# Optimization experiments

Measured on AMD Instinct MI355X. Metric: run time of the kernel, lower is better.

The kernel has to match this reference:

```python
import jax, jax.numpy as jnp
import numpy as np
import math

K = 30   # neighbors
T = 9    # num_kernel

def sparsemax(z):
    # sparsemax along last axis
    zs = jnp.sort(z, axis=-1)[..., ::-1]
    rng = jnp.arange(1, z.shape[-1] + 1, dtype=z.dtype)
    cs = jnp.cumsum(zs, axis=-1)
    support = (1.0 + rng * zs) > cs
    kz = jnp.sum(support, axis=-1, keepdims=True)
    tau = (jnp.take_along_axis(cs, kz - 1, axis=-1) - 1.0) / kz.astype(z.dtype)
    return jnp.maximum(z - tau, 0.0)

def bn(x, g, b, axes, eps=1e-5):
    # batch-norm (training-mode batch stats), channel axis = 1
    m = jnp.mean(x, axes, keepdims=True)
    v = jnp.var(x, axes, keepdims=True)
    sh = [1] * x.ndim; sh[1] = -1
    return (x - m) / jnp.sqrt(v + eps) * g.reshape(sh) + b.reshape(sh)

def _forward(x, B_ff, mlp_W, permx, W1, b1, S1, W2, b2, S2, W3, b3, S3, W4, b4, S4,
             W5, g5, be5, L1, g6, be6, L2, bL2, g7, be7, L3, bL3):
    Bsz, _, N = x.shape
    pts = jnp.transpose(x, (0, 2, 1))                      # [B,N,3]
    # knn (DGCNN-style): negative squared distance, top-k (self first)
    xx = jnp.sum(pts * pts, -1)                            # [B,N]
    inner = jnp.einsum('bnc,bmc->bnm', pts, pts)
    negd = 2.0 * inner - xx[:, :, None] - xx[:, None, :]
    _, idx = jax.lax.top_k(negd, K)                        # [B,N,K] int32
    gather = jax.vmap(lambda f, i: f[i])                   # [B,N,F],[B,N,K]->[B,N,K,F]
    # Fourier features -> sparsemax basis weights -> per-point permatrix
    ng = gather(pts, idx)                                  # [B,N,K,3]
    xrep = jnp.broadcast_to(ng[:, :, :1, :], ng.shape)     # self repeated
    rel = ng - xrep
    sq = jnp.sum(rel * rel, -1, keepdims=True)
    dist = jnp.where(sq > 0, jnp.sqrt(jnp.where(sq > 0, sq, 1.0)), 0.0)  # safe norm
    feats = jnp.concatenate([xrep, rel, dist], -1).reshape(Bsz, N, 7 * K)
    ff = (2.0 * math.pi) * (feats @ B_ff)                  # [B,N,32]
    ff = jnp.concatenate([jnp.sin(ff), jnp.cos(ff)], -1)   # [B,N,64]
    w = sparsemax(ff @ mlp_W)                              # [B,N,16]
    P = jnp.einsum('bni,ikt->bnkt', w, permx)              # [B,N,K,T]

    def paiconv(f, W, b, S):  # f: [B,Cin,N]
        ft = jnp.transpose(f, (0, 2, 1))                   # [B,N,Cin]
        nb = gather(ft, idx)                               # [B,N,K,Cin]
        agg = jnp.einsum('bnkc,bnkt->bntc', nb, P).reshape(Bsz, N, -1)
        out = agg @ W + b + ft @ S                         # [B,N,Cout]
        return jnp.transpose(out, (0, 2, 1))

    gelu = lambda a: jax.nn.gelu(a, approximate=False)
    x1 = gelu(paiconv(x,  W1, b1, S1))
    x2 = gelu(paiconv(x1, W2, b2, S2))
    x3 = gelu(paiconv(x2, W3, b3, S3))
    x4 = gelu(paiconv(x3, W4, b4, S4))
    f = jnp.concatenate([x1, x2, x3, x4], 1)               # [B,512,N]
    f = jnp.einsum('bcn,ce->ben', f, W5)                   # conv5 (1x1)
    f = gelu(bn(f, g5, be5, (0, 2)))
    h = jnp.concatenate([jnp.max(f, -1), jnp.mean(f, -1)], -1)  # [B,2048]
    h = gelu(bn(h @ L1, g6, be6, (0,)))
    h = gelu(bn(h @ L2 + bL2, g7, be7, (0,)))
    return h @ L3 + bL3


def setup_inputs() -> dict:
    key = jax.random.key(0)
    ks = jax.random.split(key, 20)
    rn = lambda k_, sh, s=1.0: jax.random.normal(k_, sh, dtype=jnp.float32) * s
    B, N = 16, 1024
    inp = {}
    inp['x'] = rn(ks[0], (B, 3, N))
    inp['B_ff'] = rn(ks[1], (7 * K, 32))
    inp['mlp_W'] = rn(ks[2], (64, 16), 0.125)
    inp['permx'] = rn(ks[3], (16, K, T), 0.1)
    dims = [(3, 64), (64, 64), (64, 128), (128, 256)]
    for i, (ci, co) in enumerate(dims, 1):
        inp['W%d' % i] = rn(ks[3 + i], (T * ci, co), 1.0 / float(np.sqrt(T * ci)))
        inp['b%d' % i] = jnp.zeros((co,), jnp.float32)
        inp['S%d' % i] = rn(ks[7 + i], (ci, co), 1.0 / float(np.sqrt(ci)))
    inp['W5'] = rn(ks[12], (512, 1024), 1.0 / float(np.sqrt(512)))
    inp['g5'] = jnp.ones((1024,), jnp.float32); inp['be5'] = jnp.zeros((1024,), jnp.float32)
    inp['L1'] = rn(ks[13], (2048, 512), 1.0 / float(np.sqrt(2048)))
    inp['g6'] = jnp.ones((512,), jnp.float32); inp['be6'] = jnp.zeros((512,), jnp.float32)
    inp['L2'] = rn(ks[14], (512, 256), 1.0 / float(np.sqrt(512))); inp['bL2'] = jnp.zeros((256,), jnp.float32)
    inp['g7'] = jnp.ones((256,), jnp.float32); inp['be7'] = jnp.zeros((256,), jnp.float32)
    inp['L3'] = rn(ks[15], (256, 40), 1.0 / float(np.sqrt(256))); inp['bL3'] = jnp.zeros((40,), jnp.float32)
    return inp


def reference(x, B_ff, mlp_W, permx, W1, b1, S1, W2, b2, S2, W3, b3, S3, W4, b4, S4,
              W5, g5, be5, L1, g6, be6, L2, bL2, g7, be7, L3, bL3):
    return _forward(x, B_ff, mlp_W, permx, W1, b1, S1, W2, b2, S2, W3, b3, S3, W4, b4, S4,
                    W5, g5, be5, L1, g6, be6, L2, bL2, g7, be7, L3, bL3)
```

## Files before the change

### kernel.cpp

```cpp
#include <hip/hip_runtime.h>
#include <hip/hip_bf16.h>
#include <cstddef>

#define BSZ 16
#define NPT 1024
#define KNN 30
#define TKR 9
#define FLT_BIG 3.402823466e+38f

typedef unsigned short u16;
typedef __attribute__((ext_vector_type(8))) u16 u16x8;
typedef __attribute__((ext_vector_type(4))) float f32x4;

__device__ __forceinline__ float gelu_f(float x) {
    return 0.5f * x * (1.0f + erff(x * 0.7071067811865476f));
}

__device__ __forceinline__ u16 bf16_rne(float a) {
    unsigned u = __float_as_uint(a);
    u += 0x7FFFu + ((u >> 16) & 1u);
    return (u16)(u >> 16);
}
__device__ __forceinline__ float bf16_tof(u16 h) {
    return __uint_as_float(((unsigned)h) << 16);
}
__device__ __forceinline__ void split_bf16(float a, u16& h, u16& l) {
    h = bf16_rne(a);
    float r = a - bf16_tof(h);
    l = bf16_rne(r);
}

__device__ __forceinline__ size_t pack_off(int row, int k, int npanels_row) {
    return (size_t)((k >> 5) * npanels_row + (row >> 7)) * 4096
         + (size_t)(((k >> 3) & 3) * 1024 + (row & 127) * 8 + (k & 7));
}

__global__ __launch_bounds__(256) void prep_all(
    const float* __restrict__ x, float* __restrict__ pts,
    const float* __restrict__ W1, const float* __restrict__ S1, float* __restrict__ wz1,
    const float* __restrict__ W2, const float* __restrict__ S2, float* __restrict__ wz2,
    const float* __restrict__ W3, const float* __restrict__ S3, float* __restrict__ wz3,
    const float* __restrict__ W4, const float* __restrict__ S4,
    u16* __restrict__ w4tH, u16* __restrict__ w4tL) {
    int layer = blockIdx.y;
    int t = blockIdx.x * 256 + threadIdx.x;
    if (layer == 0) {
        if (t >= BSZ * NPT) return;
        int b = t >> 10, n = t & 1023;
        const float* xp = x + (size_t)b * 3 * NPT;
        pts[t * 3 + 0] = xp[n];
        pts[t * 3 + 1] = xp[NPT + n];
        pts[t * 3 + 2] = xp[2 * NPT + n];
        return;
    }
    if (layer == 4) {
        if (t >= 1280 * 256) return;
        int k = t >> 8, n = t & 255;
        float v = (k < 1152) ? W4[(size_t)k * 256 + n] : S4[(size_t)(k - 1152) * 256 + n];
        u16 h, l;
        split_bf16(v, h, l);
        size_t off = pack_off(n, k, 2);
        w4tH[off] = h;
        w4tL[off] = l;
        return;
    }
    const float *W, *S; float* WZ; int KW, KS, N, kpad;
    if (layer == 1)      { W = W1; S = S1; WZ = wz1; KW = 27;   KS = 3;   N = 64;  kpad = 32;  }
    else if (layer == 2) { W = W2; S = S2; WZ = wz2; KW = 576;  KS = 64;  N = 64;  kpad = 640; }
    else                 { W = W3; S = S3; WZ = wz3; KW = 576;  KS = 64;  N = 128; kpad = 640; }
    if (t >= kpad * N) return;
    int k = t / N, n = t - k * N;
    float v = 0.0f;
    if (k < KW) v = W[(size_t)k * N + n];
    else if (k < KW + KS) v = S[(size_t)(k - KW) * N + n];
    WZ[t] = v;
}

__global__ __launch_bounds__(256) void knn_basis_kernel(
    const float* __restrict__ pts, const float* __restrict__ B_ff,
    const float* __restrict__ mlp_W, const float* __restrict__ permx,
    int* __restrict__ idx, float* __restrict__ P) {
    __shared__ float npt[4][KNN * 3];
    __shared__ float feats[4][7 * KNN];
    __shared__ float sc[4][64];
    __shared__ float zl[4][16];
    __shared__ float w[4][16];
    __shared__ float sZs[4][16];
    __shared__ float sCs[4][16];
    __shared__ int sIds[4][KNN];
    int tid = threadIdx.x;
    int wave = tid >> 6, lane = tid & 63;
    int bn_ = blockIdx.x * 4 + wave;
    int b = bn_ >> 10;

    {
        double px = (double)pts[(size_t)bn_ * 3 + 0];
        double py = (double)pts[(size_t)bn_ * 3 + 1];
        double pz = (double)pts[(size_t)bn_ * 3 + 2];
        double xn = px * px + py * py + pz * pz;
        const float* pb = pts + (size_t)(b << 10) * 3;
        int base = lane * 16;
        unsigned mono[16];
        #pragma unroll
        for (int j = 0; j < 16; j++) {
            int m = base + j;
            double qx = (double)pb[m * 3 + 0];
            double qy = (double)pb[m * 3 + 1];
            double qz = (double)pb[m * 3 + 2];
            double inner = px * qx + py * qy + pz * qz;
            double xm = qx * qx + qy * qy + qz * qz;
            double cd = 2.0 * inner - xn - xm;
            float cf = (float)cd;
            unsigned bb = __float_as_uint(cf);
            mono[j] = (bb & 0x80000000u) ? ~bb : (bb | 0x80000000u);
        }
        unsigned alive = 0xFFFFu;
        unsigned c1v = 0u, c2v = 0u;
        int c1j = 0, c2j = 0;
        #pragma unroll
        for (int j = 0; j < 16; j++) {
            unsigned v = mono[j];
            if (v > c1v) { c2v = c1v; c2j = c1j; c1v = v; c1j = j; }
            else if (v > c2v) { c2v = v; c2j = j; }
        }
        bool have2 = true;
        for (int it = 0; it < KNN; it++) {
            unsigned m = c1v;
            #pragma unroll
            for (int s = 1; s < 64; s <<= 1) {
                unsigned ov = (unsigned)__shfl_xor((int)m, s, 64);
                m = (ov > m) ? ov : m;
            }
            unsigned long long ball = __ballot(c1v == m);
            int wlan = (int)__builtin_ctzll(ball);
            int jw = __shfl(c1j, wlan, 64);
            int bi = (wlan << 4) + jw;
            if (lane == it) sIds[wave][it] = bi;
            if (lane == wlan) {
                alive &= ~(1u << c1j);
                if (have2) {
                    c1v = c2v; c1j = c2j; have2 = false;
                } else {
                    unsigned a1 = 0u, a2 = 0u;
                    int j1 = 0, j2 = 0;
                    #pragma unroll
                    for (int j = 0; j < 16; j++) {
                        unsigned v = ((alive >> j) & 1u) ? mono[j] : 0u;
                        if (v > a1) { a2 = a1; j2 = j1; a1 = v; j1 = j; }
                        else if (v > a2) { a2 = v; j2 = j; }
                    }
                    c1v = a1; c1j = j1; c2v = a2; c2j = j2;
                    have2 = true;
                }
            }
        }
        __builtin_amdgcn_wave_barrier();
        if (lane < KNN) idx[(size_t)bn_ * KNN + lane] = sIds[wave][lane];
    }
    __syncthreads();

    if (lane < KNN) {
        int m = sIds[wave][lane];
        const float* q = pts + ((size_t)(b << 10) + m) * 3;
        npt[wave][lane * 3 + 0] = q[0];
        npt[wave][lane * 3 + 1] = q[1];
        npt[wave][lane * 3 + 2] = q[2];
    }
    __syncthreads();
    if (lane < KNN) {
        float sx = npt[wave][0], sy = npt[wave][1], sz = npt[wave][2];
        float rx = npt[wave][lane * 3 + 0] - sx;
        float ry = npt[wave][lane * 3 + 1] - sy;
        float rz = npt[wave][lane * 3 + 2] - sz;
        float sq = rx * rx + ry * ry + rz * rz;
        float dist = (sq > 0.0f) ? sqrtf(sq) : 0.0f;
        feats[wave][lane * 7 + 0] = sx;
        feats[wave][lane * 7 + 1] = sy;
        feats[wave][lane * 7 + 2] = sz;
        feats[wave][lane * 7 + 3] = rx;
        feats[wave][lane * 7 + 4] = ry;
        feats[wave][lane * 7 + 5] = rz;
        feats[wave][lane * 7 + 6] = dist;
    }
    __syncthreads();
    {
        int j = lane & 31;
        int half = lane >> 5;
        int i0 = half * 105;
        float acc = 0.0f;
        for (int i = i0; i < i0 + 105; i++) acc += feats[wave][i] * B_ff[i * 32 + j];
        acc += __shfl_xor(acc, 32, 64);
        if (half == 0) {
            float ffv = 6.283185307179586f * acc;
            sc[wave][j] = sinf(ffv);
            sc[wave][j + 32] = cosf(ffv);
        }
    }
    __syncthreads();
    {
        int j = lane & 15;
        int h = lane >> 4;
        float acc = 0.0f;
        for (int i = 16 * h; i < 16 * h + 16; i++) acc += sc[wave][i] * mlp_W[i * 16 + j];
        acc += __shfl_xor(acc, 16, 64);
        acc += __shfl_xor(acc, 32, 64);
        if (h == 0) zl[wave][j] = acc;
    }
    __syncthreads();
    {
        int l = lane & 15;
        float zv = zl[wave][l];
        int rank = 0;
        #pragma unroll
        for (int j = 0; j < 16; j++) {
            float zj = zl[wave][j];
            rank += (zj > zv || (zj == zv && j < l)) ? 1 : 0;
        }
        if (lane < 16) sZs[wave][rank] = zv;
        __builtin_amdgcn_wave_barrier();
        float cs = 0.0f;
        #pragma unroll
        for (int p = 0; p < 16; p++) {
            float zp = sZs[wave][p];
            cs += (p <= l) ? zp : 0.0f;
        }
        float zsl = sZs[wave][l];
        bool flag = (lane < 16) && (1.0f + (float)(l + 1) * zsl > cs);
        unsigned long long ball = __ballot(flag);
        int cnt = (int)__popcll(ball & 0xFFFFull);
        if (lane < 16) sCs[wave][l] = cs;
        __builtin_amdgcn_wave_barrier();
        float tau = (sCs[wave][cnt - 1] - 1.0f) / (float)cnt;
        if (lane < 16) w[wave][l] = fmaxf(zv - tau, 0.0f);
    }
    __syncthreads();
    float* Pp = P + (size_t)bn_ * (KNN * TKR);
    for (int e = lane; e < KNN * TKR; e += 64) {
        int k = e / TKR, t = e - TKR * k;
        float acc = 0.0f;
        for (int i = 0; i < 16; i++) acc += w[wave][i] * permx[(i * KNN + k) * TKR + t];
        Pp[e] = acc;
    }
}

template <int CIN>
__global__ __launch_bounds__(256) void agg_kernel(
    const float* __restrict__ ft, int ftst,
    const float* __restrict__ P, const int* __restrict__ idx,
    float* __restrict__ Z, int kpad) {
    __shared__ float sP[KNN * TKR];
    __shared__ float sNb[KNN * CIN];
    __shared__ int sIdx[KNN];
    int bn_ = blockIdx.x;
    int b = bn_ >> 10;
    int tid = threadIdx.x;
    if (tid < KNN) sIdx[tid] = idx[(size_t)bn_ * KNN + tid];
    for (int e = tid; e < KNN * TKR; e += 256) sP[e] = P[(size_t)bn_ * (KNN * TKR) + e];
    __syncthreads();
    for (int e = tid; e < KNN * CIN; e += 256) {
        int k = e / CIN, c = e - k * CIN;
        sNb[e] = ft[((size_t)(b << 10) + sIdx[k]) * ftst + c];
    }
    __syncthreads();
    float* zp = Z + (size_t)bn_ * kpad;
    const int KW = TKR * CIN;
    for (int e = tid; e < kpad; e += 256) {
        float v;
        if (e < KW) {
            int t = e / CIN, c = e - t * CIN;
            float acc = 0.0f;
            #pragma unroll
            for (int k = 0; k < KNN; k++) acc += sNb[k * CIN + c] * sP[k * TKR + t];
            v = acc;
        } else if (e < KW + CIN) {
            v = ft[(size_t)bn_ * ftst + (e - KW)];
        } else {
            v = 0.0f;
        }
        zp[e] = v;
    }
}

template <int CIN>
__global__ __launch_bounds__(256) void agg_v_kernel(
    const float* __restrict__ ft, int ftst,
    const float* __restrict__ P, const int* __restrict__ idx,
    float* __restrict__ Z, int kpad) {
    __shared__ float sP[KNN * TKR];
    __shared__ float sNb[KNN * CIN];
    __shared__ int sIdx[KNN];
    constexpr int C4 = CIN / 4;
    int bn_ = blockIdx.x;
    int b = bn_ >> 10;
    int tid = threadIdx.x;
    if (tid < KNN) sIdx[tid] = idx[(size_t)bn_ * KNN + tid];
    for (int e = tid; e < KNN * TKR; e += 256) sP[e] = P[(size_t)bn_ * (KNN * TKR) + e];
    __syncthreads();
    for (int e = tid; e < KNN * C4; e += 256) {
        int k = e / C4, c4 = (e - k * C4) * 4;
        *(float4*)&sNb[k * CIN + c4] =
            *(const float4*)&ft[((size_t)(b << 10) + sIdx[k]) * ftst + c4];
    }
    __syncthreads();
    float* zp = Z + (size_t)bn_ * kpad;
    const int KW = TKR * CIN;
    for (int e = tid; e < (kpad >> 2); e += 256) {
        int c0 = e * 4;
        float4 v;
        if (c0 < KW) {
            int t = c0 / CIN, c4 = c0 - t * CIN;
            float4 a = make_float4(0.f, 0.f, 0.f, 0.f);
            #pragma unroll
            for (int k = 0; k < KNN; k++) {
                float p = sP[k * TKR + t];
                float4 nb = *(const float4*)&sNb[k * CIN + c4];
                a.x += nb.x * p; a.y += nb.y * p;
                a.z += nb.z * p; a.w += nb.w * p;
            }
            v = a;
        } else if (c0 < KW + CIN) {
            v = *(const float4*)&ft[(size_t)bn_ * ftst + (c0 - KW)];
        } else {
            v = make_float4(0.f, 0.f, 0.f, 0.f);
        }
        *(float4*)&zp[c0] = v;
    }
}

__global__ __launch_bounds__(256) void agg_v_split8_kernel(
    const float* __restrict__ ft, int ftst,
    const float* __restrict__ P, const int* __restrict__ idx,
    u16* __restrict__ ZH, u16* __restrict__ ZL) {
    __shared__ int   sIdx8[8][KNN];
    __shared__ float sP8[8][KNN * TKR];
    __shared__ __align__(16) u16 oH[8][1288];
    __shared__ __align__(16) u16 oL[8][1288];
    int tid = threadIdx.x;
    int row = tid >> 5;
    int cq = tid & 31;
    int c0 = cq << 2;
    int r0 = blockIdx.x << 3;
    int b = r0 >> 10;

    if (tid < 8 * KNN) {
        int r = tid / KNN, k = tid - r * KNN;
        sIdx8[r][k] = idx[(size_t)(r0 + r) * KNN + k];
    }
    for (int e = tid; e < 8 * KNN * TKR; e += 256) {
        int r = e / (KNN * TKR), i = e - r * (KNN * TKR);
        sP8[r][i] = P[(size_t)(r0 + r) * (KNN * TKR) + i];
    }
    __syncthreads();

    float4 acc[9];
    #pragma unroll
    for (int t = 0; t < 9; t++) acc[t] = make_float4(0.f, 0.f, 0.f, 0.f);
    const float* fb = ft + (size_t)(b << 10) * ftst;
    for (int k = 0; k < KNN; k++) {
        float4 nb = *(const float4*)&fb[(size_t)sIdx8[row][k] * ftst + c0];
        #pragma unroll
        for (int t = 0; t < 9; t++) {
            float p = sP8[row][k * TKR + t];
            acc[t].x += nb.x * p; acc[t].y += nb.y * p;
            acc[t].z += nb.z * p; acc[t].w += nb.w * p;
        }
    }
    float4 self = *(const float4*)&ft[(size_t)(r0 + row) * ftst + c0];

    #pragma unroll
    for (int t = 0; t < 10; t++) {
        float4 v = (t < 9) ? acc[t] : self;
        int e0 = (t < 9) ? (t * 128 + c0) : (1152 + c0);
        u16 h[4], l[4];
        split_bf16(v.x, h[0], l[0]);
        split_bf16(v.y, h[1], l[1]);
        split_bf16(v.z, h[2], l[2]);
        split_bf16(v.w, h[3], l[3]);
        uint2 hv, lv;
        hv.x = (unsigned)h[0] | ((unsigned)h[1] << 16);
        hv.y = (unsigned)h[2] | ((unsigned)h[3] << 16);
        lv.x = (unsigned)l[0] | ((unsigned)l[1] << 16);
        lv.y = (unsigned)l[2] | ((unsigned)l[3] << 16);
        *(uint2*)&oH[row][e0] = hv;
        *(uint2*)&oL[row][e0] = lv;
    }
    __syncthreads();

    for (int u = tid; u < 2560; u += 256) {
        int kp = u >> 6;
        int l = u & 63;
        int kc = l >> 4, rg = (l >> 3) & 1, rw = (l >> 1) & 3, half = l & 1;
        int rloc = rg * 4 + rw;
        int eloc = kp * 32 + kc * 8 + half * 4;
        uint2 hv = *(const uint2*)&oH[rloc][eloc];
        uint2 lv = *(const uint2*)&oL[rloc][eloc];
        size_t off = (size_t)(kp * 128 + (r0 >> 7)) * 4096
                   + (size_t)(kc * 1024 + ((r0 & 127) + rloc) * 8 + half * 4);
        *(uint2*)&ZH[off] = hv;
        *(uint2*)&ZL[off] = lv;
    }
}

template <bool GELU, bool HASBIAS>
__global__ __launch_bounds__(256) void gemm_f32_64db(
    const float* __restrict__ A, int lda,
    const float* __restrict__ B, int ldb, int K,
    const float* __restrict__ bias,
    float* __restrict__ C, int ldc) {
    __shared__ float As[2][16][64];
    __shared__ float Bs[2][16][64];
    int tid = threadIdx.x;
    int tx = tid & 15, ty = tid >> 4;
    int m0 = blockIdx.y * 64, n0 = blockIdx.x * 64;
    float acc[4][4];
    #pragma unroll
    for (int i = 0; i < 4; i++)
        #pragma unroll
        for (int j = 0; j < 4; j++) acc[i][j] = 0.0f;

    int ar = tid >> 2, ac0 = (tid & 3) * 4;
    const float* aptr = A + (size_t)(m0 + ar) * lda + ac0;
    int br = tid >> 4, bc = (tid & 15) * 4;
    const float* bptr = B + (size_t)br * ldb + n0 + bc;

    float4 pa = *(const float4*)(aptr);
    float4 pb = *(const float4*)(bptr);
    As[0][ac0 + 0][ar] = pa.x; As[0][ac0 + 1][ar] = pa.y;
    As[0][ac0 + 2][ar] = pa.z; As[0][ac0 + 3][ar] = pa.w;
    *(float4*)&Bs[0][br][bc] = pb;
    __syncthreads();

    int nk = K >> 4;
    for (int t = 0; t < nk; t++) {
        int buf = t & 1;
        bool more = (t + 1) < nk;
        if (more) {
            int k0 = (t + 1) << 4;
            pa = *(const float4*)(aptr + k0);
            pb = *(const float4*)(bptr + (size_t)k0 * ldb);
        }
        #pragma unroll
        for (int kk = 0; kk < 16; kk++) {
            float av[4], bv[4];
            *(float4*)&av[0] = *(const float4*)&As[buf][kk][ty * 4];
            *(float4*)&bv[0] = *(const float4*)&Bs[buf][kk][tx * 4];
            #pragma unroll
            for (int i = 0; i < 4; i++)
                #pragma unroll
                for (int j = 0; j < 4; j++) acc[i][j] += av[i] * bv[j];
        }
        if (more) {
            int nb = 1 - buf;
            As[nb][ac0 + 0][ar] = pa.x; As[nb][ac0 + 1][ar] = pa.y;
            As[nb][ac0 + 2][ar] = pa.z; As[nb][ac0 + 3][ar] = pa.w;
            *(float4*)&Bs[nb][br][bc] = pb;
        }
        __syncthreads();
    }
    #pragma unroll
    for (int i = 0; i < 4; i++) {
        int r = m0 + ty * 4 + i;
        int c = n0 + tx * 4;
        float v[4];
        #pragma unroll
        for (int j = 0; j < 4; j++) {
            float t = acc[i][j];
            if (HASBIAS) t += bias[c + j];
            if (GELU) t = gelu_f(t);
            v[j] = t;
        }
        *(float4*)(C + (size_t)r * ldc + c) = *(float4*)v;
    }
}

__global__ __launch_bounds__(256) void convert_split(
    const float* __restrict__ feat, u16* __restrict__ fH, u16* __restrict__ fL,
    const float* __restrict__ W5, u16* __restrict__ wH, u16* __restrict__ wL) {
    int t = blockIdx.x * 256 + threadIdx.x;
    if (blockIdx.y == 0) {
        int T = t >> 9, s = t & 511;
        int kc = s >> 7, rloc = s & 127;
        int kp = T >> 7, rp = T & 127;
        int row = (rp << 7) + rloc;
        int k0 = (kp << 5) + (kc << 3);
        const float* fp = &feat[(size_t)row * 512 + k0];
        float4 a = *(const float4*)fp;
        float4 b = *(const float4*)(fp + 4);
        float v[8] = {a.x, a.y, a.z, a.w, b.x, b.y, b.z, b.w};
        u16 h[8], l[8];
        #pragma unroll
        for (int i = 0; i < 8; i++) split_bf16(v[i], h[i], l[i]);
        uint4 hv, lv;
        hv.x = (unsigned)h[0] | ((unsigned)h[1] << 16);
        hv.y = (unsigned)h[2] | ((unsigned)h[3] << 16);
        hv.z = (unsigned)h[4] | ((unsigned)h[5] << 16);
        hv.w = (unsigned)h[6] | ((unsigned)h[7] << 16);
        lv.x = (unsigned)l[0] | ((unsigned)l[1] << 16);
        lv.y = (unsigned)l[2] | ((unsigned)l[3] << 16);
        lv.z = (unsigned)l[4] | ((unsigned)l[5] << 16);
        lv.w = (unsigned)l[6] | ((unsigned)l[7] << 16);
        size_t off = (size_t)T * 4096 + kc * 1024 + rloc * 8;
        *(uint4*)&fH[off] = hv;
        *(uint4*)&fL[off] = lv;
    } else {
        if (t >= 512 * 1024) return;
        int n = t >> 9, k = t & 511;
        u16 h, l;
        split_bf16(W5[(size_t)k * 1024 + n], h, l);
        size_t off = pack_off(n, k, 8);
        wH[off] = h; wL[off] = l;
    }
}

template <bool STATS, bool GELU, bool HASBIAS>
__global__ __launch_bounds__(256) void mfma_bf16x3(
    const u16* __restrict__ fH, const u16* __restrict__ fL,
    const u16* __restrict__ wH, const u16* __restrict__ wL,
    int K, const float* __restrict__ bias,
    float* __restrict__ C, int ldc,
    float* __restrict__ partS, float* __restrict__ partQ) {
    __shared__ __align__(16) u16 lds[2][16384];
    int tid = threadIdx.x;
    int lane = tid & 63, wave = tid >> 6;
    int wr = wave >> 1, wc = wave & 1;
    int kg = lane >> 4, r = lane & 15;

    int nwg = gridDim.x * gridDim.y;
    int hw = blockIdx.y * gridDim.x + blockIdx.x;
    int logical = (hw & 7) * (nwg >> 3) + (hw >> 3);
    int nb = logical % gridDim.x;
    int mb = logical / gridDim.x;
    int m0 = mb << 7, n0 = nb << 7;
    int nmp = gridDim.y;
    int nnp = gridDim.x;

    const u16* src = (wave == 0) ? fH : (wave == 1) ? fL
                   : (wave == 2) ? wH : wL;

    f32x4 acc[4][4];
    #pragma unroll
    for (int i = 0; i < 4; i++)
        #pragma unroll
        for (int j = 0; j < 4; j++) {
            acc[i][j][0] = 0.0f; acc[i][j][1] = 0.0f;
            acc[i][j][2] = 0.0f; acc[i][j][3] = 0.0f;
        }

#define STAGE_K(BUF, TT) {                                                     \
    size_t tb = ((size_t)((wave < 2) ? ((TT) * nmp + mb)                       \
                                     : ((TT) * nnp + nb)) << 12);              \
    _Pragma("unroll")                                                          \
    for (int iw = 0; iw < 8; iw++) {                                           \
        const u16* gp = src + tb + (size_t)(((iw << 6) + lane) << 3);          \
        __builtin_amdgcn_global_load_lds(                                      \
            (const __attribute__((address_space(1))) void*)gp,                 \
            (__attribute__((address_space(3))) void*)&lds[BUF][(wave << 12) + (iw << 9)], \
            16, 0, 0);                                                         \
    } }

    int nk = K >> 5;
    STAGE_K(0, 0);
    __syncthreads();
    for (int t = 0; t < nk; t++) {
        if (t + 1 < nk) STAGE_K((t + 1) & 1, (t + 1));
        const u16* lb = lds[t & 1];
        u16x8 bh[4], bl[4];
        #pragma unroll
        for (int fj = 0; fj < 4; fj++) {
            int bcol = (wc << 6) + (fj << 4) + r;
            bh[fj] = *(const u16x8*)&lb[ 8192 + (((kg << 7) + bcol) << 3)];
            bl[fj] = *(const u16x8*)&lb[12288 + (((kg << 7) + bcol) << 3)];
        }
        #pragma unroll
        for (int fi = 0; fi < 4; fi++) {
            int arow = (wr << 6) + (fi << 4) + r;
            u16x8 ah = *(const u16x8*)&lb[       (((kg << 7) + arow) << 3)];
            u16x8 al = *(const u16x8*)&lb[4096 + (((kg << 7) + arow) << 3)];
            #pragma unroll
            for (int fj = 0; fj < 4; fj++) {
                asm volatile("v_mfma_f32_16x16x32_bf16 %0, %1, %2, %0"
                             : "+v"(acc[fi][fj]) : "v"(ah), "v"(bh[fj]));
                asm volatile("v_mfma_f32_16x16x32_bf16 %0, %1, %2, %0"
                             : "+v"(acc[fi][fj]) : "v"(ah), "v"(bl[fj]));
                asm volatile("v_mfma_f32_16x16x32_bf16 %0, %1, %2, %0"
                             : "+v"(acc[fi][fj]) : "v"(al), "v"(bh[fj]));
            }
        }
        __syncthreads();
    }
#undef STAGE_K

    asm volatile("s_nop 15\n\ts_nop 15" ::: "memory");

    float bvv[4];
    if (HASBIAS) {
        #pragma unroll
        for (int fj = 0; fj < 4; fj++) bvv[fj] = bias[n0 + (wc << 6) + (fj << 4) + r];
    }

    #pragma unroll
    for (int fi = 0; fi < 4; fi++)
        #pragma unroll
        for (int ri = 0; ri < 4; ri++) {
            int row = m0 + (wr << 6) + (fi << 4) + (kg << 2) + ri;
            float* cp = C + (size_t)row * ldc + n0 + (wc << 6) + r;
            #pragma unroll
            for (int fj = 0; fj < 4; fj++) {
                float v = acc[fi][fj][ri];
                if (HASBIAS) v += bvv[fj];
                if (GELU) v = gelu_f(v);
                cp[fj << 4] = v;
            }
        }

    if (STATS) {
        __syncthreads();
        float* sS = (float*)lds;
        float* sQ = sS + 1024;
        int slot = (wr << 2) + kg;
        #pragma unroll
        for (int fj = 0; fj < 4; fj++) {
            float s = 0.0f, q = 0.0f;
            #pragma unroll
            for (int fi = 0; fi < 4; fi++)
                #pragma unroll
                for (int ri = 0; ri < 4; ri++) {
                    float v = acc[fi][fj][ri];
                    s += v; q += v * v;
                }
            int cl = (wc << 6) + (fj << 4) + r;
            sS[slot * 128 + cl] = s;
            sQ[slot * 128 + cl] = q;
        }
        __syncthreads();
        if (tid < 128) {
            float S = 0.0f, Q = 0.0f;
            #pragma unroll
            for (int i = 0; i < 8; i++) { S += sS[i * 128 + tid]; Q += sQ[i * 128 + tid]; }
            partS[(size_t)mb * 1024 + n0 + tid] = S;
            partQ[(size_t)mb * 1024 + n0 + tid] = Q;
        }
    }
}

__global__ __launch_bounds__(256) void stats_reduce(
    const float* __restrict__ partS, const float* __restrict__ partQ,
    const float* __restrict__ g, const float* __restrict__ be,
    float* __restrict__ scaleb, float* __restrict__ shiftb) {
    int e = blockIdx.x * 256 + threadIdx.x;
    if (e >= 1024) return;
    double s = 0.0, q = 0.0;
    for (int mb = 0; mb < 128; mb++) {
        s += (double)partS[(size_t)mb * 1024 + e];
        q += (double)partQ[(size_t)mb * 1024 + e];
    }
    double m = s * (1.0 / 16384.0);
    double v = q * (1.0 / 16384.0) - m * m;
    float sc = g[e] * (float)(1.0 / sqrt(v + 1e-5));
    scaleb[e] = sc;
    shiftb[e] = be[e] - (float)m * sc;
}

__global__ __launch_bounds__(256) void pool_partial(
    const float* __restrict__ f5, const float* __restrict__ scaleb,
    const float* __restrict__ shiftb,
    float* __restrict__ partM, double* __restrict__ partSd) {
    int chunk = blockIdx.x, g = blockIdx.y, b = blockIdx.z;
    int tid = threadIdx.x;
    int lane = tid & 63, nlane = tid >> 6;
    int c0 = (g << 8) + lane * 4;
    float4 sc = *(const float4*)&scaleb[c0];
    float4 sh = *(const float4*)&shiftb[c0];
    float m0 = -FLT_BIG, m1 = -FLT_BIG, m2 = -FLT_BIG, m3 = -FLT_BIG;
    double s0 = 0.0, s1 = 0.0, s2 = 0.0, s3 = 0.0;
    int nend = (chunk + 1) << 6;
    for (int n = (chunk << 6) + nlane; n < nend; n += 4) {
        float4 v = *(const float4*)&f5[((size_t)(b << 10) + n) * 1024 + c0];
        float g0 = gelu_f(v.x * sc.x + sh.x);
        float g1 = gelu_f(v.y * sc.y + sh.y);
        float g2 = gelu_f(v.z * sc.z + sh.z);
        float g3 = gelu_f(v.w * sc.w + sh.w);
        m0 = fmaxf(m0, g0); m1 = fmaxf(m1, g1);
        m2 = fmaxf(m2, g2); m3 = fmaxf(m3, g3);
        s0 += (double)g0; s1 += (double)g1;
        s2 += (double)g2; s3 += (double)g3;
    }
    __shared__ float smax[4][256];
    __shared__ double ssum[4][256];
    *(float4*)&smax[nlane][lane * 4] = make_float4(m0, m1, m2, m3);
    ssum[nlane][lane * 4 + 0] = s0;
    ssum[nlane][lane * 4 + 1] = s1;
    ssum[nlane][lane * 4 + 2] = s2;
    ssum[nlane][lane * 4 + 3] = s3;
    __syncthreads();
    if (nlane == 0) {
        size_t base = ((size_t)((b * 4 + g) * 16 + chunk)) * 256 + lane * 4;
        #pragma unroll
        for (int j = 0; j < 4; j++) {
            float mm = smax[0][lane * 4 + j];
            double ss = ssum[0][lane * 4 + j];
            #pragma unroll
            for (int i = 1; i < 4; i++) {
                mm = fmaxf(mm, smax[i][lane * 4 + j]);
                ss += ssum[i][lane * 4 + j];
            }
            partM[base + j] = mm;
            partSd[base + j] = ss;
        }
    }
}

__global__ __launch_bounds__(256) void pool_finish(
    const float* __restrict__ partM, const double* __restrict__ partSd,
    float* __restrict__ h) {
    int b = blockIdx.x;
    int e0 = threadIdx.x * 4;
    int g = e0 >> 8, cl = e0 & 255;
    float mm[4] = {-FLT_BIG, -FLT_BIG, -FLT_BIG, -FLT_BIG};
    double ss[4] = {0.0, 0.0, 0.0, 0.0};
    for (int chunk = 0; chunk < 16; chunk++) {
        size_t base = ((size_t)((b * 4 + g) * 16 + chunk)) * 256 + cl;
        float4 pm = *(const float4*)&partM[base];
        mm[0] = fmaxf(mm[0], pm.x); mm[1] = fmaxf(mm[1], pm.y);
        mm[2] = fmaxf(mm[2], pm.z); mm[3] = fmaxf(mm[3], pm.w);
        ss[0] += partSd[base + 0]; ss[1] += partSd[base + 1];
        ss[2] += partSd[base + 2]; ss[3] += partSd[base + 3];
    }
    #pragma unroll
    for (int j = 0; j < 4; j++) {
        h[(size_t)b * 2048 + e0 + j] = mm[j];
        h[(size_t)b * 2048 + 1024 + e0 + j] = (float)(ss[j] * (1.0 / 1024.0));
    }
}

__global__ __launch_bounds__(256) void fc_split(
    const float* __restrict__ X, const float* __restrict__ W,
    double* __restrict__ part, int Bn, int In, int Out, int KC) {
    int tid = blockIdx.x * 256 + threadIdx.x;
    if (tid >= Bn * Out * KC) return;
    int chunk = tid / (Bn * Out);
    int r = tid - chunk * (Bn * Out);
    int b = r / Out, j = r - b * Out;
    int len = In / KC;
    int i0 = chunk * len;
    const float* x = X + (size_t)b * In + i0;
    const float* w = W + (size_t)i0 * Out + j;
    double acc = 0.0;
    for (int i = 0; i < len; i++) acc += (double)x[i] * (double)w[(size_t)i * Out];
    part[tid] = acc;
}

__global__ __launch_bounds__(256) void fc_bn_gelu(
    const double* __restrict__ part, const float* __restrict__ bias,
    const float* __restrict__ g, const float* __restrict__ be,
    float* __restrict__ Y, int Out, int KC) {
    int j = blockIdx.x * 256 + threadIdx.x;
    if (j >= Out) return;
    float r[BSZ];
    for (int b = 0; b < BSZ; b++) {
        double acc = bias ? (double)bias[j] : 0.0;
        for (int c = 0; c < KC; c++) acc += part[(size_t)c * (BSZ * Out) + b * Out + j];
        r[b] = (float)acc;
    }
    double m = 0.0;
    for (int b = 0; b < BSZ; b++) m += (double)r[b];
    m /= (double)BSZ;
    double v = 0.0;
    for (int b = 0; b < BSZ; b++) {
        double dd = (double)r[b] - m;
        v += dd * dd;
    }
    v /= (double)BSZ;
    float sc = g[j] * (float)(1.0 / sqrt(v + 1e-5));
    float sh = be[j] - (float)m * sc;
    for (int b = 0; b < BSZ; b++) Y[b * Out + j] = gelu_f(r[b] * sc + sh);
}

__global__ __launch_bounds__(256) void fc_reduce(
    const double* __restrict__ part, const float* __restrict__ bias,
    float* __restrict__ Y, int Bn, int Out, int KC) {
    int r = blockIdx.x * 256 + threadIdx.x;
    if (r >= Bn * Out) return;
    int j = r % Out;
    double acc = bias ? (double)bias[j] : 0.0;
    for (int c = 0; c < KC; c++) acc += part[(size_t)c * (Bn * Out) + r];
    Y[r] = (float)acc;
}

extern "C" void kernel_launch(void* const* d_in, const int* in_sizes, int n_in,
                              void* d_out, int out_size, void* d_ws, size_t ws_size,
                              hipStream_t stream) {
    const float* x     = (const float*)d_in[0];
    const float* B_ff  = (const float*)d_in[1];
    const float* mlp_W = (const float*)d_in[2];
    const float* permx = (const float*)d_in[3];
    const float* W1 = (const float*)d_in[4];
    const float* b1 = (const float*)d_in[5];
    const float* S1 = (const float*)d_in[6];
    const float* W2 = (const float*)d_in[7];
    const float* b2 = (const float*)d_in[8];
    const float* S2 = (const float*)d_in[9];
    const float* W3 = (const float*)d_in[10];
    const float* b3 = (const float*)d_in[11];
    const float* S3 = (const float*)d_in[12];
    const float* W4 = (const float*)d_in[13];
    const float* b4 = (const float*)d_in[14];
    const float* S4 = (const float*)d_in[15];
    const float* W5 = (const float*)d_in[16];
    const float* g5 = (const float*)d_in[17];
    const float* be5 = (const float*)d_in[18];
    const float* L1 = (const float*)d_in[19];
    const float* g6 = (const float*)d_in[20];
    const float* be6 = (const float*)d_in[21];
    const float* L2 = (const float*)d_in[22];
    const float* bL2 = (const float*)d_in[23];
    const float* g7 = (const float*)d_in[24];
    const float* be7 = (const float*)d_in[25];
    const float* L3 = (const float*)d_in[26];
    const float* bL3 = (const float*)d_in[27];
    float* outp = (float*)d_out;

    const int BN = BSZ * NPT;

    float* ws = (float*)d_ws;
    float* pts   = ws;
    int*   idxb  = (int*)(ws + 49152);
    float* Pb    = ws + 540672;
    float* feat  = Pb + 4423680;
    float* Zbig  = feat + 8388608;
    u16*   ZH    = (u16*)Zbig;
    u16*   ZL    = (u16*)(Zbig + 10485760);
    float* f5    = Zbig;
    u16*   featH = (u16*)(Zbig + 16777216);
    float* poolM = Zbig + 16777216;
    double* poolS = (double*)(Zbig + 16777216 + 262144);
    float* w4slot = Zbig + 20971520;
    u16*   w4tH  = (u16*)w4slot;
    u16*   w4tL  = w4tH + 327680;
    float* scb   = w4slot + 327680;
    float* shb   = scb + 1024;
    float* hb    = shb + 1024;
    float* y1    = hb + 32768;
    float* y2    = y1 + 8192;
    float* partC_S = y2 + 4096;
    float* partC_Q = partC_S + 131072;
    double* partF  = (double*)(partC_Q + 131072);
    float* wsend = (float*)(partF + 131072);
    u16* featL = (u16*)ws;
    u16* w5tH  = (u16*)(ws + 4194304);
    u16* w5tL  = (u16*)(ws + 4456448);
    float* wz1   = Zbig + 11010048;
    float* wz2   = wz1 + 2048;
    float* wz3   = wz2 + 40960;
    size_t need_bytes = (size_t)(wsend - ws) * sizeof(float);
    if (ws_size < need_bytes) return;

    prep_all<<<dim3(1280, 5), 256, 0, stream>>>(
        x, pts, W1, S1, wz1, W2, S2, wz2, W3, S3, wz3, W4, S4, w4tH, w4tL);

    knn_basis_kernel<<<BN / 4, 256, 0, stream>>>(pts, B_ff, mlp_W, permx, idxb, Pb);

    agg_kernel<3><<<BN, 256, 0, stream>>>(pts, 3, Pb, idxb, Zbig, 32);
    gemm_f32_64db<true, true><<<dim3(1, 256), 256, 0, stream>>>(
        Zbig, 32, wz1, 64, 32, b1, feat + 0, 512);
    agg_v_kernel<64><<<BN, 256, 0, stream>>>(feat + 0, 512, Pb, idxb, Zbig, 640);
    gemm_f32_64db<true, true><<<dim3(1, 256), 256, 0, stream>>>(
        Zbig, 640, wz2, 64, 640, b2, feat + 64, 512);
    agg_v_kernel<64><<<BN, 256, 0, stream>>>(feat + 64, 512, Pb, idxb, Zbig, 640);
    gemm_f32_64db<true, true><<<dim3(2, 256), 256, 0, stream>>>(
        Zbig, 640, wz3, 128, 640, b3, feat + 128, 512);
    agg_v_split8_kernel<<<BN / 8, 256, 0, stream>>>(feat + 128, 512, Pb, idxb, ZH, ZL);
    mfma_bf16x3<false, true, true><<<dim3(2, 128), 256, 0, stream>>>(
        ZH, ZL, w4tH, w4tL, 1280, b4, feat + 256, 512, nullptr, nullptr);

    convert_split<<<dim3(4096, 2), 256, 0, stream>>>(feat, featH, featL, W5, w5tH, w5tL);
    mfma_bf16x3<true, false, false><<<dim3(8, 128), 256, 0, stream>>>(
        featH, featL, w5tH, w5tL, 512, nullptr, f5, 1024, partC_S, partC_Q);

    stats_reduce<<<4, 256, 0, stream>>>(partC_S, partC_Q, g5, be5, scb, shb);
    pool_partial<<<dim3(16, 4, BSZ), 256, 0, stream>>>(f5, scb, shb, poolM, poolS);
    pool_finish<<<BSZ, 256, 0, stream>>>(poolM, poolS, hb);

    fc_split<<<(BSZ * 512 * 16 + 255) / 256, 256, 0, stream>>>(hb, L1, partF, BSZ, 2048, 512, 16);
    fc_bn_gelu<<<2, 256, 0, stream>>>(partF, nullptr, g6, be6, y1, 512, 16);
    fc_split<<<(BSZ * 256 * 8 + 255) / 256, 256, 0, stream>>>(y1, L2, partF, BSZ, 512, 256, 8);
    fc_bn_gelu<<<1, 256, 0, stream>>>(partF, bL2, g7, be7, y2, 256, 8);
    fc_split<<<(BSZ * 40 * 4 + 255) / 256, 256, 0, stream>>>(y2, L3, partF, BSZ, 256, 40, 4);
    fc_reduce<<<(BSZ * 40 + 255) / 256, 256, 0, stream>>>(partF, bL3, outp, BSZ, 40, 4);
}
```

Before: 690.6 us.

## Move layer 2/3 PAI convolutions to split-bf16 MFMA GEMM with packed aggregation

Layers 2 and 3 now use the bf16x3 MFMA GEMM instead of the fp32 scalar GEMM. A new aggregation kernel handles 8 points per block, splits each result into high and low bf16 parts, and writes them directly in the MFMA panel layout. The layer 2/3 weights are pre-split and packed in prep_all, padded to 128 columns, and the MFMA kernel gains a bias bound for the padded columns. The aim is to replace slow fp32 GEMMs with matrix-core math while keeping near-fp32 accuracy. The cost is extra split and pack work, plus wasted compute on the padded columns of layer 2, whose zero output spills into the next layer's slots before they are overwritten.

After: 656.2 us, median of 2. 1.05x faster.

```diff
diff --git a/kernel.cpp b/kernel.cpp
--- a/kernel.cpp
+++ b/kernel.cpp
@@ -38,8 +38,10 @@
 __global__ __launch_bounds__(256) void prep_all(
     const float* __restrict__ x, float* __restrict__ pts,
     const float* __restrict__ W1, const float* __restrict__ S1, float* __restrict__ wz1,
-    const float* __restrict__ W2, const float* __restrict__ S2, float* __restrict__ wz2,
-    const float* __restrict__ W3, const float* __restrict__ S3, float* __restrict__ wz3,
+    const float* __restrict__ W2, const float* __restrict__ S2,
+    u16* __restrict__ w2tH, u16* __restrict__ w2tL,
+    const float* __restrict__ W3, const float* __restrict__ S3,
+    u16* __restrict__ w3tH, u16* __restrict__ w3tL,
     const float* __restrict__ W4, const float* __restrict__ S4,
     u16* __restrict__ w4tH, u16* __restrict__ w4tL) {
     int layer = blockIdx.y;
@@ -53,27 +55,38 @@
         pts[t * 3 + 2] = xp[2 * NPT + n];
         return;
     }
-    if (layer == 4) {
-        if (t >= 1280 * 256) return;
-        int k = t >> 8, n = t & 255;
-        float v = (k < 1152) ? W4[(size_t)k * 256 + n] : S4[(size_t)(k - 1152) * 256 + n];
+    if (layer == 1) {
+        if (t >= 32 * 64) return;
+        int k = t >> 6, n = t & 63;
+        float v = 0.0f;
+        if (k < 27) v = W1[(size_t)k * 64 + n];
+        else if (k < 30) v = S1[(size_t)(k - 27) * 64 + n];
+        wz1[t] = v;
+        return;
+    }
+    if (layer == 2 || layer == 3) {
+        if (t >= 640 * 128) return;
+        int k = t >> 7, n = t & 127;
+        const float* W = (layer == 2) ? W2 : W3;
+        const float* S = (layer == 2) ? S2 : S3;
+        int N = (layer == 2) ? 64 : 128;
+        float v = 0.0f;
+        if (n < N) v = (k < 576) ? W[(size_t)k * N + n] : S[(size_t)(k - 576) * N + n];
         u16 h, l;
         split_bf16(v, h, l);
-        size_t off = pack_off(n, k, 2);
-        w4tH[off] = h;
-        w4tL[off] = l;
+        size_t off = pack_off(n, k, 1);
+        if (layer == 2) { w2tH[off] = h; w2tL[off] = l; }
+        else            { w3tH[off] = h; w3tL[off] = l; }
         return;
     }
-    const float *W, *S; float* WZ; int KW, KS, N, kpad;
-    if (layer == 1)      { W = W1; S = S1; WZ = wz1; KW = 27;   KS = 3;   N = 64;  kpad = 32;  }
-    else if (layer == 2) { W = W2; S = S2; WZ = wz2; KW = 576;  KS = 64;  N = 64;  kpad = 640; }
-    else                 { W = W3; S = S3; WZ = wz3; KW = 576;  KS = 64;  N = 128; kpad = 640; }
-    if (t >= kpad * N) return;
-    int k = t / N, n = t - k * N;
-    float v = 0.0f;
-    if (k < KW) v = W[(size_t)k * N + n];
-    else if (k < KW + KS) v = S[(size_t)(k - KW) * N + n];
-    WZ[t] = v;
+    if (t >= 1280 * 256) return;
+    int k = t >> 8, n = t & 255;
+    float v = (k < 1152) ? W4[(size_t)k * 256 + n] : S4[(size_t)(k - 1152) * 256 + n];
+    u16 h, l;
+    split_bf16(v, h, l);
+    size_t off = pack_off(n, k, 2);
+    w4tH[off] = h;
+    w4tL[off] = l;
 }
 
 __global__ __launch_bounds__(256) void knn_basis_kernel(
@@ -281,49 +294,61 @@
     }
 }
 
-template <int CIN>
-__global__ __launch_bounds__(256) void agg_v_kernel(
+__global__ __launch_bounds__(256) void agg_v_split_c64_kernel(
     const float* __restrict__ ft, int ftst,
     const float* __restrict__ P, const int* __restrict__ idx,
-    float* __restrict__ Z, int kpad) {
-    __shared__ float sP[KNN * TKR];
-    __shared__ float sNb[KNN * CIN];
-    __shared__ int sIdx[KNN];
-    constexpr int C4 = CIN / 4;
-    int bn_ = blockIdx.x;
-    int b = bn_ >> 10;
+    u16* __restrict__ ZH, u16* __restrict__ ZL) {
+    __shared__ int   sIdx8[8][KNN];
+    __shared__ float sP8[8][KNN * TKR];
+    __shared__ __align__(16) u16 oH[8][644];
+    __shared__ __align__(16) u16 oL[8][644];
     int tid = threadIdx.x;
-    if (tid < KNN) sIdx[tid] = idx[(size_t)bn_ * KNN + tid];
-    for (int e = tid; e < KNN * TKR; e += 256) sP[e] = P[(size_t)bn_ * (KNN * TKR) + e];
-    __syncthreads();
-    for (int e = tid; e < KNN * C4; e += 256) {
-        int k = e / C4, c4 = (e - k * C4) * 4;
-        *(float4*)&sNb[k * CIN + c4] =
-            *(const float4*)&ft[((size_t)(b << 10) + sIdx[k]) * ftst + c4];
-    }
-    __syncthreads();
-    float* zp = Z + (size_t)bn_ * kpad;
-    const int KW = TKR * CIN;
-    for (int e = tid; e < (kpad >> 2); e += 256) {
-        int c0 = e * 4;
-        float4 v;
-        if (c0 < KW) {
-            int t = c0 / CIN, c4 = c0 - t * CIN;
-            float4 a = make_float4(0.f, 0.f, 0.f, 0.f);
-            #pragma unroll
-            for (int k = 0; k < KNN; k++) {
-                float p = sP[k * TKR + t];
-                float4 nb = *(const float4*)&sNb[k * CIN + c4];
-                a.x += nb.x * p; a.y += nb.y * p;
-                a.z += nb.z * p; a.w += nb.w * p;
-            }
-            v = a;
-        } else if (c0 < KW + CIN) {
-            v = *(const float4*)&ft[(size_t)bn_ * ftst + (c0 - KW)];
-        } else {
-            v = make_float4(0.f, 0.f, 0.f, 0.f);
-        }
-        *(float4*)&zp[c0] = v;
+    int row = tid >> 5, cp = tid & 31, c0 = cp << 1;
+    int r0 = blockIdx.x << 3;
+    int b = r0 >> 10;
+    if (tid < 8 * KNN) {
+        int r = tid / KNN, k = tid - r * KNN;
+        sIdx8[r][k] = idx[(size_t)(r0 + r) * KNN + k];
+    }
+    for (int e = tid; e < 8 * KNN * TKR; e += 256) {
+        int r = e / (KNN * TKR), i = e - r * (KNN * TKR);
+        sP8[r][i] = P[(size_t)(r0 + r) * (KNN * TKR) + i];
+    }
+    __syncthreads();
+    float2 acc[9];
+    #pragma unroll
+    for (int t = 0; t < 9; t++) acc[t] = make_float2(0.f, 0.f);
+    const float* fb = ft + (size_t)(b << 10) * ftst;
+    for (int k = 0; k < KNN; k++) {
+        float2 nb = *(const float2*)&fb[(size_t)sIdx8[row][k] * ftst + c0];
+        #pragma unroll
+        for (int t = 0; t < 9; t++) {
+            float p = sP8[row][k * TKR + t];
+            acc[t].x += nb.x * p; acc[t].y += nb.y * p;
+        }
+    }
+    float2 self = *(const float2*)&ft[(size_t)(r0 + row) * ftst + c0];
+    #pragma unroll
+    for (int t = 0; t < 10; t++) {
+        float2 v = (t < 9) ? acc[t] : self;
+        int e0 = (t < 9) ? (t * 64 + c0) : (576 + c0);
+        u16 h0, l0, h1, l1;
+        split_bf16(v.x, h0, l0);
+        split_bf16(v.y, h1, l1);
+        *(unsigned*)&oH[row][e0] = (unsigned)h0 | ((unsigned)h1 << 16);
+        *(unsigned*)&oL[row][e0] = (unsigned)l0 | ((unsigned)l1 << 16);
+    }
+    __syncthreads();
+    for (int u = tid; u < 1280; u += 256) {
+        int kp = u >> 6, s = u & 63;
+        int kc = s >> 4, rloc = (s >> 1) & 7, half = s & 1;
+        int eloc = kp * 32 + kc * 8 + half * 4;
+        uint2 hv = *(const uint2*)&oH[rloc][eloc];
+        uint2 lv = *(const uint2*)&oL[rloc][eloc];
+        size_t off = (size_t)(kp * 128 + (r0 >> 7)) * 4096
+                   + (size_t)(kc * 1024 + ((r0 & 127) + rloc) * 8 + half * 4);
+        *(uint2*)&ZH[off] = hv;
+        *(uint2*)&ZL[off] = lv;
     }
 }
 
@@ -516,7 +541,7 @@
 __global__ __launch_bounds__(256) void mfma_bf16x3(
     const u16* __restrict__ fH, const u16* __restrict__ fL,
     const u16* __restrict__ wH, const u16* __restrict__ wL,
-    int K, const float* __restrict__ bias,
+    int K, const float* __restrict__ bias, int nbias,
     float* __restrict__ C, int ldc,
     float* __restrict__ partS, float* __restrict__ partQ) {
     __shared__ __align__(16) u16 lds[2][16384];
@@ -595,7 +620,10 @@
     float bvv[4];
     if (HASBIAS) {
         #pragma unroll
-        for (int fj = 0; fj < 4; fj++) bvv[fj] = bias[n0 + (wc << 6) + (fj << 4) + r];
+        for (int fj = 0; fj < 4; fj++) {
+            int col = n0 + (wc << 6) + (fj << 4) + r;
+            bvv[fj] = (col < nbias) ? bias[col] : 0.0f;
+        }
     }
 
     #pragma unroll
@@ -845,37 +873,41 @@
     float* partC_S = y2 + 4096;
     float* partC_Q = partC_S + 131072;
     double* partF  = (double*)(partC_Q + 131072);
-    float* wsend = (float*)(partF + 131072);
+    float* extra = (float*)(partF + 131072);
+    u16* w2tH = (u16*)extra;
+    u16* w2tL = w2tH + 81920;
+    u16* w3tH = w2tL + 81920;
+    u16* w3tL = w3tH + 81920;
+    float* wz1 = extra + 163840;
+    float* wsend = wz1 + 2048;
     u16* featL = (u16*)ws;
     u16* w5tH  = (u16*)(ws + 4194304);
     u16* w5tL  = (u16*)(ws + 4456448);
-    float* wz1   = Zbig + 11010048;
-    float* wz2   = wz1 + 2048;
-    float* wz3   = wz2 + 40960;
     size_t need_bytes = (size_t)(wsend - ws) * sizeof(float);
     if (ws_size < need_bytes) return;
 
     prep_all<<<dim3(1280, 5), 256, 0, stream>>>(
-        x, pts, W1, S1, wz1, W2, S2, wz2, W3, S3, wz3, W4, S4, w4tH, w4tL);
+        x, pts, W1, S1, wz1, W2, S2, w2tH, w2tL, W3, S3, w3tH, w3tL,
+        W4, S4, w4tH, w4tL);
 
     knn_basis_kernel<<<BN / 4, 256, 0, stream>>>(pts, B_ff, mlp_W, permx, idxb, Pb);
 
     agg_kernel<3><<<BN, 256, 0, stream>>>(pts, 3, Pb, idxb, Zbig, 32);
     gemm_f32_64db<true, true><<<dim3(1, 256), 256, 0, stream>>>(
         Zbig, 32, wz1, 64, 32, b1, feat + 0, 512);
-    agg_v_kernel<64><<<BN, 256, 0, stream>>>(feat + 0, 512, Pb, idxb, Zbig, 640);
-    gemm_f32_64db<true, true><<<dim3(1, 256), 256, 0, stream>>>(
-        Zbig, 640, wz2, 64, 640, b2, feat + 64, 512);
-    agg_v_kernel<64><<<BN, 256, 0, stream>>>(feat + 64, 512, Pb, idxb, Zbig, 640);
-    gemm_f32_64db<true, true><<<dim3(2, 256), 256, 0, stream>>>(
-        Zbig, 640, wz3, 128, 640, b3, feat + 128, 512);
+    agg_v_split_c64_kernel<<<BN / 8, 256, 0, stream>>>(feat + 0, 512, Pb, idxb, ZH, ZL);
+    mfma_bf16x3<false, true, true><<<dim3(1, 128), 256, 0, stream>>>(
+        ZH, ZL, w2tH, w2tL, 640, b2, 64, feat + 64, 512, nullptr, nullptr);
+    agg_v_split_c64_kernel<<<BN / 8, 256, 0, stream>>>(feat + 64, 512, Pb, idxb, ZH, ZL);
+    mfma_bf16x3<false, true, true><<<dim3(1, 128), 256, 0, stream>>>(
+        ZH, ZL, w3tH, w3tL, 640, b3, 128, feat + 128, 512, nullptr, nullptr);
     agg_v_split8_kernel<<<BN / 8, 256, 0, stream>>>(feat + 128, 512, Pb, idxb, ZH, ZL);
     mfma_bf16x3<false, true, true><<<dim3(2, 128), 256, 0, stream>>>(
-        ZH, ZL, w4tH, w4tL, 1280, b4, feat + 256, 512, nullptr, nullptr);
+        ZH, ZL, w4tH, w4tL, 1280, b4, 256, feat + 256, 512, nullptr, nullptr);
 
     convert_split<<<dim3(4096, 2), 256, 0, stream>>>(feat, featH, featL, W5, w5tH, w5tL);
     mfma_bf16x3<true, false, false><<<dim3(8, 128), 256, 0, stream>>>(
-        featH, featL, w5tH, w5tL, 512, nullptr, f5, 1024, partC_S, partC_Q);
+        featH, featL, w5tH, w5tL, 512, nullptr, 0, f5, 1024, partC_S, partC_Q);
 
     stats_reduce<<<4, 256, 0, stream>>>(partC_S, partC_Q, g5, be5, scb, shb);
     pool_partial<<<dim3(16, 4, BSZ), 256, 0, stream>>>(f5, scb, shb, poolM, poolS);
```
